# Kernel tuning notes

Hardware: AMD Instinct MI355X
Metric: run time of the kernel (lower is better)

## Reference

```python
import jax, jax.numpy as jnp
import numpy as np

B, R, C = 2, 64, 256
PH = PW = 7
KMAX = 8            # max pool-kernel size per axis given roi size bounds (kernel<=7 here)
HW = [160, 80, 40, 20]   # FPN level spatial sizes for a 640px image, strides 4/8/16/32
STRIDES = [4.0, 8.0, 16.0, 32.0]
TOP = 224.0         # config.top_pyramid_roi_size
HIDDEN = 2048
NCLS = 20
SCALE = float(np.round(np.sqrt(C), 2))  # np.round(sqrt(inner_dim),2) in SelfAttention


def setup_inputs() -> dict:
    key = jax.random.key(0)
    ks = jax.random.split(key, 32)
    U = lambda k, s, lo, hi: jax.random.uniform(k, s, minval=lo, maxval=hi)
    x1 = U(ks[0], (B, R), 0.0, 260.0)
    y1 = U(ks[1], (B, R), 0.0, 260.0)
    w = U(ks[2], (B, R), 16.0, 360.0)
    h = U(ks[3], (B, R), 16.0, 360.0)
    rois = jnp.stack([x1, y1, jnp.minimum(x1 + w, 639.0), jnp.minimum(y1 + h, 639.0)], -1)
    N = lambda k, s, sc: (sc * jax.random.normal(k, s)).astype(jnp.float32)
    inp = {'rois': rois}
    for i in range(4):
        inp[f'fm{i}'] = N(ks[4 + i], (B, C, HW[i], HW[i]), 1.0)
    inp['wq'] = N(ks[8], (C, C), 0.02);  inp['bq'] = jnp.zeros((C,), jnp.float32)
    inp['wk'] = N(ks[9], (C, C), 0.02);  inp['bk'] = jnp.zeros((C,), jnp.float32)
    inp['wv'] = N(ks[10], (C, C), 0.02); inp['bv'] = jnp.zeros((C,), jnp.float32)
    inp['wo'] = N(ks[11], (C, C), 0.02); inp['bo'] = jnp.zeros((C,), jnp.float32)
    inp['w1'] = N(ks[12], (C * PH * PW, HIDDEN), 0.02); inp['b1'] = jnp.zeros((HIDDEN,), jnp.float32)
    inp['w2'] = N(ks[13], (HIDDEN, HIDDEN), 0.02);       inp['b2'] = jnp.zeros((HIDDEN,), jnp.float32)
    inp['wreg'] = N(ks[14], (HIDDEN, 4 * (NCLS + 1)), 0.02); inp['breg'] = jnp.zeros((4 * (NCLS + 1),), jnp.float32)
    inp['wcls'] = N(ks[15], (HIDDEN, NCLS + 1), 0.02);       inp['bcls'] = jnp.zeros((NCLS + 1,), jnp.float32)
    return inp


def _forward(rois, fm0, fm1, fm2, fm3, wq, bq, wk, bk, wv, bv, wo, bo,
             w1, b1, w2, b2, wreg, breg, wcls, bcls):
    Hmax = HW[0]
    pad = lambda fm: jnp.pad(fm, ((0, 0), (0, 0), (0, Hmax - fm.shape[-2]), (0, Hmax - fm.shape[-1])))
    feats = jnp.stack([pad(fm0), pad(fm1), pad(fm2), pad(fm3)])  # [4,B,C,Hmax,Hmax]
    heights = jnp.array(HW, jnp.int32)
    strides = jnp.array(STRIDES, jnp.float32)

    r = rois.reshape(-1, 4)                 # [N,4] xyxy in pixels
    Nroi = r.shape[0]
    bidx = jnp.repeat(jnp.arange(B, dtype=jnp.int32), R)
    size = jnp.sqrt((r[:, 2] - r[:, 0]) * (r[:, 3] - r[:, 1]))
    # int() truncates toward zero, then clamp(0,3) -- matches torch
    lvl = jnp.clip((3.0 + jnp.log(size / TOP)).astype(jnp.int32), 0, 3)
    s = strides[lvl]
    x1 = (r[:, 0] / s).astype(jnp.int32); y1 = (r[:, 1] / s).astype(jnp.int32)
    x2 = (r[:, 2] / s).astype(jnp.int32); y2 = (r[:, 3] / s).astype(jnp.int32)
    Hl = heights[lvl]                        # per-roi level map size (square maps)

    def expand(lo, hi, cap, pool):
        # replicate the symmetric while-loop expansion until span >= pool
        for _ in range(pool):
            need = (hi - lo + 1) < pool
            lo = jnp.where(need, jnp.maximum(lo - 1, 0), lo)
            hi = jnp.where(need, jnp.minimum(hi + 1, cap - 1), hi)
        return lo, hi

    y1, y2 = expand(y1, y2, Hl, PH)
    x1, x2 = expand(x1, x2, Hl, PW)
    rh = y2 - y1 + 1; rw = x2 - x1 + 1
    kh = (rh + PH - 1) // PH; sh = rh // PH   # ceil / floor kernel & stride
    kw = (rw + PW - 1) // PW; sw = rw // PW

    ar_p = jnp.arange(PH); ar_k = jnp.arange(KMAX)

    def pool_one(l, b, yy, xx, kh_, kw_, sh_, sw_):
        rows = jnp.clip(yy + ar_p[:, None] * sh_ + ar_k[None, :], 0, Hmax - 1)  # [PH,K]
        cols = jnp.clip(xx + ar_p[:, None] * sw_ + ar_k[None, :], 0, Hmax - 1)  # [PW,K]
        patch = feats[l, b][:, rows[:, :, None, None], cols[None, None, :, :]]  # [C,PH,K,PW,K]
        m = (ar_k < kh_)[:, None, None] & (ar_k < kw_)[None, None, :]           # [K,1,K] -> bcast
        patch = jnp.where(m, patch, -jnp.inf)
        return patch.max(axis=(2, 4))                                           # [C,PH,PW]

    pooled = jax.vmap(pool_one)(lvl, bidx, y1, x1, kh, kw, sh, sw)  # [N,C,PH,PW]

    # SelfAttention over the PH*PW spatial tokens of each ROI
    L = PH * PW
    tok = pooled.reshape(Nroi, C, L).transpose(0, 2, 1)            # [N,L,C]
    q = tok @ wq + bq
    k = tok @ wk + bk
    v = tok @ wv + bv
    att = jax.nn.softmax(jnp.einsum('nlc,nmc->nlm', q, k) / SCALE, axis=-1)
    ctx = jnp.einsum('nlm,nmc->nlc', att, v) @ wo + bo             # [N,L,C]
    x = pooled.reshape(Nroi, C, L) + ctx.transpose(0, 2, 1)        # residual add
    x = x.reshape(Nroi, C * L)

    h1 = jax.nn.relu(x @ w1 + b1)
    h2 = jax.nn.relu(h1 @ w2 + b2)
    bbox_reg = h2 @ wreg + breg                                    # [N, 4*(NCLS+1)]
    bbox_classes = jax.nn.softmax(h2 @ wcls + bcls, axis=-1)       # [N, NCLS+1]
    return bbox_reg, bbox_classes


def reference(rois, fm0, fm1, fm2, fm3, wq, bq, wk, bk, wv, bv, wo, bo,
              w1, b1, w2, b2, wreg, breg, wcls, bcls):
    return _forward(rois, fm0, fm1, fm2, fm3, wq, bq, wk, bk, wv, bv, wo, bo,
                    w1, b1, w2, b2, wreg, breg, wcls, bcls)
```

## Files before the change

### kernel.cpp

```cpp
#include <hip/hip_runtime.h>
#include <hip/hip_bf16.h>
#include <stdint.h>

typedef __attribute__((ext_vector_type(8))) short bf16x8;
typedef __attribute__((ext_vector_type(4))) float f32x4;

__device__ __forceinline__ float blo(unsigned u){ union{float f;unsigned x;}v; v.x = u<<16; return v.f; }
__device__ __forceinline__ float bhi(unsigned u){ union{float f;unsigned x;}v; v.x = u & 0xFFFF0000u; return v.f; }
__device__ __forceinline__ unsigned short f2bf(float f){
  union{float f;unsigned x;}v; v.f=f; unsigned x=v.x;
  return (unsigned short)((x + 0x7fffu + ((x>>16)&1u)) >> 16);
}
__device__ __forceinline__ unsigned cvtpk(float lo, float hi){
  unsigned r;
  asm("v_cvt_pk_bf16_f32 %0, %1, %2" : "=v"(r) : "v"(lo), "v"(hi));
  return r;
}

__global__ __launch_bounds__(256) void pool_pack_kernel(
    const float* __restrict__ rois,
    const float* __restrict__ fm0, const float* __restrict__ fm1,
    const float* __restrict__ fm2, const float* __restrict__ fm3,
    float* __restrict__ pooled, unsigned short* __restrict__ tok,
    const float* __restrict__ wreg, const float* __restrict__ wcls, float* __restrict__ wT)
{
  int bx = blockIdx.x;
  int tid = threadIdx.x;
  if (bx >= 896){
    int c = bx - 896;
    if (c < 84){
      for (int k = tid; k < 2048; k += 256) wT[(size_t)c*2048 + k] = wreg[(size_t)k*84 + c];
    } else {
      int cc = c - 84;
      for (int k = tid; k < 2048; k += 256) wT[(size_t)c*2048 + k] = wcls[(size_t)k*21 + cc];
    }
    return;
  }
  int n = bx / 7;
  int ph = bx - n*7;
  int c = tid;
  const float* r = rois + n*4;
  int b = n >> 6;
  float rx1=r[0], ry1=r[1], rx2=r[2], ry2=r[3];
  float size = sqrtf((rx2-rx1)*(ry2-ry1));
  int lvl = (int)(3.0f + logf(size/224.0f));
  if (lvl < 0) lvl = 0; if (lvl > 3) lvl = 3;
  const float strides_[4] = {4.f,8.f,16.f,32.f};
  const int hw_[4] = {160,80,40,20};
  float s = strides_[lvl]; int Hl = hw_[lvl];
  int x1 = (int)(rx1/s), y1 = (int)(ry1/s), x2 = (int)(rx2/s), y2 = (int)(ry2/s);
  #pragma unroll
  for (int it=0; it<7; ++it){
    bool need = (y2-y1+1) < 7;
    if (need){ y1 = (y1-1 > 0) ? y1-1 : 0; y2 = (y2+1 < Hl-1) ? y2+1 : Hl-1; }
  }
  #pragma unroll
  for (int it=0; it<7; ++it){
    bool need = (x2-x1+1) < 7;
    if (need){ x1 = (x1-1 > 0) ? x1-1 : 0; x2 = (x2+1 < Hl-1) ? x2+1 : Hl-1; }
  }
  int rh = y2-y1+1, rw = x2-x1+1;
  int kh = (rh+6)/7, sh = rh/7, kw = (rw+6)/7, sw = rw/7;
  const float* fm = (lvl==0)?fm0:(lvl==1)?fm1:(lvl==2)?fm2:fm3;
  const float* fp = fm + ((size_t)(b*256 + c))*(size_t)(Hl*Hl);
  int r0 = y1 + ph*sh;
  for (int pw=0; pw<7; ++pw){
    int c0 = x1 + pw*sw;
    float m = -3.4e38f;
    for (int i=0;i<kh;++i){
      const float* rp = fp + (size_t)(r0+i)*Hl + c0;
      for (int j=0;j<kw;++j) m = fmaxf(m, rp[j]);
    }
    int l = ph*7+pw;
    pooled[((size_t)n*256 + c)*49 + l] = m;
    tok[((size_t)n*49 + l)*256 + c] = f2bf(m);
  }
}

template<int EPI>
__global__ __launch_bounds__(256) void gemm_kernel(
    const unsigned short* __restrict__ A,
    const float* __restrict__ B0, const float* __restrict__ B1, const float* __restrict__ B2,
    const float* __restrict__ bias0, const float* __restrict__ bias1, const float* __restrict__ bias2,
    unsigned short* __restrict__ o0, unsigned short* __restrict__ o1, unsigned short* __restrict__ o2,
    float* __restrict__ outf, const float* __restrict__ pooled,
    int M, int Nper, int K, int nM, int nN, int kChunk)
{
  __shared__ __align__(16) unsigned short Bs[2][2048];
  int per = nM*nN;
  int kc  = blockIdx.x / per;
  int rem = blockIdx.x - kc*per;
  int bm = rem % nM, bn = rem / nM;
  int m0 = bm*64, n0 = bn*64;
  int mat = n0 / Nper;
  int col0 = n0 - mat*Nper;
  const float* Bp    = (mat==0)?B0:(mat==1)?B1:B2;
  const float* biasp = (mat==0)?bias0:(mat==1)?bias1:bias2;
  unsigned short* outp = (mat==0)?o0:(mat==1)?o1:o2;
  int k0 = kc*kChunk;
  int nMacro = kChunk >> 7;
  int tid = threadIdx.x, lane = tid & 63, wave = tid >> 6;
  int wm = wave & 1, wn = wave >> 1;
  int g = lane >> 4, c = lane & 15;

  f32x4 acc[2][2];
  #pragma unroll
  for (int i=0;i<2;++i)
    #pragma unroll
    for (int j=0;j<2;++j){ acc[i][j][0]=0.f; acc[i][j][1]=0.f; acc[i][j][2]=0.f; acc[i][j][3]=0.f; }

  int brow = tid >> 3, bcg = tid & 7;
  int bw_idx = brow*64 + ((bcg*8) ^ ((brow>>3)<<4));
  const float* Bbase = Bp + (size_t)brow*Nper + col0 + bcg*8;
  int rb0 = g*512 + (((wn*2  )^g)*16 + c);
  int rb1 = g*512 + (((wn*2+1)^g)*16 + c);
  const unsigned short* Ap0 = A + (size_t)(m0 + wm*32 +      c)*K + g*8;
  const unsigned short* Ap1 = A + (size_t)(m0 + wm*32 + 16 + c)*K + g*8;

  auto writeB = [&](int buf, const float4& bx, const float4& by){
    uint4 w;
    w.x = cvtpk(bx.x,bx.y); w.y = cvtpk(bx.z,bx.w);
    w.z = cvtpk(by.x,by.y); w.w = cvtpk(by.z,by.w);
    *(uint4*)&Bs[buf][bw_idx] = w;
  };
  auto readFrags = [&](int buf, bf16x8& r0, bf16x8& r1){
    union { unsigned short s[8]; bf16x8 v; } u0, u1;
    const unsigned short* bsp = &Bs[buf][0];
    #pragma unroll
    for (int j=0;j<8;++j){ u0.s[j] = bsp[rb0 + j*64]; u1.s[j] = bsp[rb1 + j*64]; }
    r0 = u0.v; r1 = u1.v;
  };
  auto mfma4 = [&](const bf16x8& f0, const bf16x8& f1, const bf16x8& q0, const bf16x8& q1){
    acc[0][0] = __builtin_amdgcn_mfma_f32_16x16x32_bf16(f0,q0,acc[0][0],0,0,0);
    acc[0][1] = __builtin_amdgcn_mfma_f32_16x16x32_bf16(f0,q1,acc[0][1],0,0,0);
    acc[1][0] = __builtin_amdgcn_mfma_f32_16x16x32_bf16(f1,q0,acc[1][0],0,0,0);
    acc[1][1] = __builtin_amdgcn_mfma_f32_16x16x32_bf16(f1,q1,acc[1][1],0,0,0);
  };

  for (int mi = 0; mi < nMacro; ++mi){
    int kk = k0 + (mi << 7);
    uint4 a0x = *(const uint4*)(Ap0+kk),    a0y = *(const uint4*)(Ap1+kk);
    uint4 a1x = *(const uint4*)(Ap0+kk+32), a1y = *(const uint4*)(Ap1+kk+32);
    uint4 a2x = *(const uint4*)(Ap0+kk+64), a2y = *(const uint4*)(Ap1+kk+64);
    uint4 a3x = *(const uint4*)(Ap0+kk+96), a3y = *(const uint4*)(Ap1+kk+96);
    const float* p0 = Bbase + (size_t)kk*Nper;
    const float* p1 = p0 + (size_t)32*Nper;
    const float* p2 = p0 + (size_t)64*Nper;
    const float* p3 = p0 + (size_t)96*Nper;
    float4 b0a = *(const float4*)p0, b0b = *(const float4*)(p0+4);
    float4 b1a = *(const float4*)p1, b1b = *(const float4*)(p1+4);
    float4 b2a = *(const float4*)p2, b2b = *(const float4*)(p2+4);
    float4 b3a = *(const float4*)p3, b3b = *(const float4*)(p3+4);

    writeB(0, b0a, b0b);
    __syncthreads();

    bf16x8 q0,q1;
    readFrags(0,q0,q1);
    writeB(1,b1a,b1b);
    mfma4(*(const bf16x8*)&a0x, *(const bf16x8*)&a0y, q0,q1);
    __syncthreads();

    readFrags(1,q0,q1);
    writeB(0,b2a,b2b);
    mfma4(*(const bf16x8*)&a1x, *(const bf16x8*)&a1y, q0,q1);
    __syncthreads();

    readFrags(0,q0,q1);
    writeB(1,b3a,b3b);
    mfma4(*(const bf16x8*)&a2x, *(const bf16x8*)&a2y, q0,q1);
    __syncthreads();

    readFrags(1,q0,q1);
    mfma4(*(const bf16x8*)&a3x, *(const bf16x8*)&a3y, q0,q1);
  }

  int rq = g << 2, cl = c;
  #pragma unroll
  for (int mr=0;mr<2;++mr){
    #pragma unroll
    for (int nc=0;nc<2;++nc){
      int rowb = m0 + wm*32 + mr*16 + rq;
      int colM = col0 + wn*32 + nc*16 + cl;
      #pragma unroll
      for (int r2=0;r2<4;++r2){
        float v = acc[mr][nc][r2];
        int rr = rowb + r2;
        if constexpr (EPI==0){
          v += biasp[colM];
          outp[(size_t)rr*Nper + colM] = f2bf(v);
        } else if constexpr (EPI==1){
          v += biasp[colM];
          int nn = rr/49, l = rr - nn*49;
          v += pooled[((size_t)nn*256 + colM)*49 + l];
          outp[(size_t)nn*12544 + colM*49 + l] = f2bf(v);
        } else {
          outf[(size_t)kc*M*Nper + (size_t)rr*Nper + colM] = v;
        }
      }
    }
  }
}

__global__ __launch_bounds__(256) void reduce1_kernel(
    const float* __restrict__ part, const float* __restrict__ b1,
    unsigned short* __restrict__ h1, int nPart)
{
  int i = blockIdx.x*256 + threadIdx.x;
  float4 s = ((const float4*)part)[i];
  for (int kc = 1; kc < nPart; ++kc){
    float4 p = ((const float4*)part)[(size_t)kc*65536 + i];
    s.x += p.x; s.y += p.y; s.z += p.z; s.w += p.w;
  }
  float4 bb = *(const float4*)(b1 + ((i<<2) & 2047));
  s.x = fmaxf(s.x+bb.x,0.f); s.y = fmaxf(s.y+bb.y,0.f);
  s.z = fmaxf(s.z+bb.z,0.f); s.w = fmaxf(s.w+bb.w,0.f);
  uint2 w;
  w.x = cvtpk(s.x, s.y); w.y = cvtpk(s.z, s.w);
  *(uint2*)&h1[(size_t)i<<2] = w;
}

__global__ __launch_bounds__(256) void reduce2_kernel(
    const float* __restrict__ part, float* __restrict__ h2f, int nPart)
{
  int i = blockIdx.x*256 + threadIdx.x;
  float4 s = ((const float4*)part)[i];
  for (int kc = 1; kc < nPart; ++kc){
    float4 p = ((const float4*)part)[(size_t)kc*65536 + i];
    s.x += p.x; s.y += p.y; s.z += p.z; s.w += p.w;
  }
  ((float4*)h2f)[i] = s;
}

__global__ __launch_bounds__(256) void attn_kernel(
    const unsigned short* __restrict__ Q, const unsigned short* __restrict__ Km,
    const unsigned short* __restrict__ V, unsigned short* __restrict__ ctx)
{
  int n = blockIdx.x, half = blockIdx.y, tid = threadIdx.x;
  int r0 = half*25, rcnt = half ? 24 : 25;
  __shared__ __align__(16) unsigned short qs[25*256];
  __shared__ __align__(16) unsigned short ks[49*260];
  __shared__ float S[25*49];
  const uint4* qg = (const uint4*)(Q + ((size_t)n*49 + r0)*256);
  for (int i = tid; i < rcnt*32; i += 256) ((uint4*)qs)[i] = qg[i];
  const uint2* kg = (const uint2*)(Km + (size_t)n*49*256);
  for (int i = tid; i < 49*64; i += 256){
    int j = i >> 6, s = i & 63;
    *(uint2*)(ks + j*260 + s*4) = kg[i];
  }
  __syncthreads();
  for (int p = tid; p < rcnt*49; p += 256){
    int i = p/49, j = p - i*49;
    const uint2* qr = (const uint2*)(qs + i*256);
    const uint2* kr = (const uint2*)(ks + j*260);
    float sum = 0.f;
    #pragma unroll 8
    for (int c4 = 0; c4 < 64; ++c4){
      uint2 qv = qr[c4], kv = kr[c4];
      sum += blo(qv.x)*blo(kv.x) + bhi(qv.x)*bhi(kv.x);
      sum += blo(qv.y)*blo(kv.y) + bhi(qv.y)*bhi(kv.y);
    }
    S[p] = sum * (1.0f/16.0f);
  }
  __syncthreads();
  const uint2* vg = (const uint2*)(V + (size_t)n*49*256);
  for (int i = tid; i < 49*64; i += 256){
    int j = i >> 6, s = i & 63;
    *(uint2*)(ks + j*260 + s*4) = vg[i];
  }
  if (tid < rcnt){
    float* row = S + tid*49;
    float mx = row[0];
    for (int j=1;j<49;++j) mx = fmaxf(mx,row[j]);
    float sm = 0.f;
    for (int j=0;j<49;++j){ float e = expf(row[j]-mx); row[j]=e; sm+=e; }
    float inv = 1.0f/sm;
    for (int j=0;j<49;++j) row[j] *= inv;
  }
  __syncthreads();
  for (int idx = tid; idx < rcnt*64; idx += 256){
    int i = idx >> 6, cp4 = idx & 63;
    const float* att = S + i*49;
    float s0=0.f, s1=0.f, s2=0.f, s3=0.f;
    #pragma unroll 7
    for (int j=0;j<49;++j){
      uint2 v = *(const uint2*)(ks + j*260 + cp4*4);
      float a = att[j];
      s0 += a*blo(v.x); s1 += a*bhi(v.x);
      s2 += a*blo(v.y); s3 += a*bhi(v.y);
    }
    uint2 outw;
    outw.x = (unsigned)f2bf(s0) | ((unsigned)f2bf(s1) << 16);
    outw.y = (unsigned)f2bf(s2) | ((unsigned)f2bf(s3) << 16);
    *(uint2*)&ctx[((size_t)n*49 + r0 + i)*256 + cp4*4] = outw;
  }
}

__global__ __launch_bounds__(256) void heads_dot(
    const float* __restrict__ h2f, const float* __restrict__ b2,
    const float* __restrict__ wT,
    const float* __restrict__ breg, const float* __restrict__ bcls,
    float* __restrict__ out, float* __restrict__ logits)
{
  int gw = (blockIdx.x*256 + threadIdx.x) >> 6;
  int lane = threadIdx.x & 63;
  int m = gw / 105, c = gw - m*105;
  const float4* hp = (const float4*)(h2f + (size_t)m*2048);
  const float4* bp = (const float4*)b2;
  const float4* wp = (const float4*)(wT + (size_t)c*2048);
  float sum = 0.f;
  #pragma unroll
  for (int i=0;i<8;++i){
    float4 a = hp[i*64 + lane];
    float4 bb = bp[i*64 + lane];
    float4 w = wp[i*64 + lane];
    sum += fmaxf(a.x+bb.x,0.f)*w.x + fmaxf(a.y+bb.y,0.f)*w.y
         + fmaxf(a.z+bb.z,0.f)*w.z + fmaxf(a.w+bb.w,0.f)*w.w;
  }
  #pragma unroll
  for (int off=32; off; off>>=1) sum += __shfl_down(sum, off, 64);
  if (lane == 0){
    if (c < 84) out[(size_t)m*84 + c] = sum + breg[c];
    else        logits[(size_t)m*21 + (c-84)] = sum + bcls[c-84];
  }
}

__global__ __launch_bounds__(128) void cls_softmax(
    const float* __restrict__ logits, float* __restrict__ out)
{
  int m = threadIdx.x;
  const float* lg = logits + (size_t)m*21;
  float mx = lg[0];
  #pragma unroll
  for (int j=1;j<21;++j) mx = fmaxf(mx, lg[j]);
  float sm = 0.f;
  float e[21];
  #pragma unroll
  for (int j=0;j<21;++j){ e[j] = expf(lg[j]-mx); sm += e[j]; }
  float inv = 1.0f/sm;
  #pragma unroll
  for (int j=0;j<21;++j) out[10752 + (size_t)m*21 + j] = e[j]*inv;
}

extern "C" void kernel_launch(void* const* d_in, const int* in_sizes, int n_in,
                              void* d_out, int out_size, void* d_ws, size_t ws_size,
                              hipStream_t stream)
{
  (void)in_sizes; (void)n_in; (void)out_size; (void)ws_size;
  const float* rois = (const float*)d_in[0];
  const float* fm0  = (const float*)d_in[1];
  const float* fm1  = (const float*)d_in[2];
  const float* fm2  = (const float*)d_in[3];
  const float* fm3  = (const float*)d_in[4];
  const float* wq   = (const float*)d_in[5];
  const float* bq   = (const float*)d_in[6];
  const float* wk   = (const float*)d_in[7];
  const float* bk   = (const float*)d_in[8];
  const float* wv   = (const float*)d_in[9];
  const float* bv   = (const float*)d_in[10];
  const float* wo   = (const float*)d_in[11];
  const float* bo   = (const float*)d_in[12];
  const float* w1   = (const float*)d_in[13];
  const float* b1   = (const float*)d_in[14];
  const float* w2   = (const float*)d_in[15];
  const float* b2   = (const float*)d_in[16];
  const float* wreg = (const float*)d_in[17];
  const float* breg = (const float*)d_in[18];
  const float* wcls = (const float*)d_in[19];
  const float* bcls = (const float*)d_in[20];
  float* out = (float*)d_out;

  char* ws = (char*)d_ws;
  float*          pooled = (float*)(ws + 0);
  unsigned short* tok    = (unsigned short*)(ws + 6422528);
  unsigned short* Qb     = (unsigned short*)(ws + 9633792);
  unsigned short* Kb     = (unsigned short*)(ws + 12845056);
  unsigned short* Vb     = (unsigned short*)(ws + 16056320);
  unsigned short* ctx    = (unsigned short*)(ws + 19267584);
  unsigned short* xb     = (unsigned short*)(ws + 22478848);
  float*          h2f    = (float*)(ws + 25690112);
  unsigned short* h1     = (unsigned short*)(ws + 26738688);
  float*          wT     = (float*)(ws + 27787264);
  float*          logits = (float*)(ws + 28647424);
  float*          h1part = (float*)(ws + 0);
  float*          h2part = (float*)(ws + 0);

  pool_pack_kernel<<<1001,256,0,stream>>>(rois, fm0, fm1, fm2, fm3, pooled, tok,
                                          wreg, wcls, wT);

  gemm_kernel<0><<<1176,256,0,stream>>>(tok, wq,wk,wv, bq,bk,bv,
                                        Qb,Kb,Vb, nullptr, nullptr, 6272,256,256, 98,12, 256);

  attn_kernel<<<dim3(128,2),256,0,stream>>>(Qb, Kb, Vb, ctx);

  gemm_kernel<1><<<392,256,0,stream>>>(ctx, wo,wo,wo, bo,bo,bo,
                                       xb,xb,xb, nullptr, pooled, 6272,256,256, 98,4, 256);

  gemm_kernel<2><<<896,256,0,stream>>>(xb, w1,w1,w1, nullptr,nullptr,nullptr,
                                       nullptr,nullptr,nullptr, h1part, nullptr,
                                       128,2048,12544, 2,32, 896);
  reduce1_kernel<<<256,256,0,stream>>>(h1part, b1, h1, 14);

  gemm_kernel<2><<<1024,256,0,stream>>>(h1, w2,w2,w2, nullptr,nullptr,nullptr,
                                        nullptr,nullptr,nullptr, h2part, nullptr,
                                        128,2048,2048, 2,32, 128);
  reduce2_kernel<<<256,256,0,stream>>>(h2part, h2f, 16);

  heads_dot<<<3360,256,0,stream>>>(h2f, b2, wT, breg, bcls, out, logits);
  cls_softmax<<<1,128,0,stream>>>(logits, out);
}
```

Baseline: 189.2 us.

## Pre-pack w1/w2 into swizzled bf16 tiles before the MLP GEMMs

```diff
diff --git a/kernel.cpp b/kernel.cpp
--- a/kernel.cpp
+++ b/kernel.cpp
@@ -22,10 +22,33 @@
     const float* __restrict__ fm0, const float* __restrict__ fm1,
     const float* __restrict__ fm2, const float* __restrict__ fm3,
     float* __restrict__ pooled, unsigned short* __restrict__ tok,
-    const float* __restrict__ wreg, const float* __restrict__ wcls, float* __restrict__ wT)
+    const float* __restrict__ wreg, const float* __restrict__ wcls, float* __restrict__ wT,
+    const float* __restrict__ w1c, unsigned short* __restrict__ w1p,
+    const float* __restrict__ w2c, unsigned short* __restrict__ w2p)
 {
   int bx = blockIdx.x;
   int tid = threadIdx.x;
+  if (bx >= 1001){
+    int cb = bx - 1001;
+    const float* W; unsigned short* P; int kb, Kp;
+    if (cb < 1568){ W = w1c; P = w1p; kb = cb*8;          Kp = 392; }
+    else          { W = w2c; P = w2p; kb = (cb-1568)*8;   Kp = 64;  }
+    int k  = kb + (tid>>5);
+    int bn = tid & 31;
+    int kr = k & 31, k32 = k >> 5;
+    const float4* src = (const float4*)(W + (size_t)k*2048 + bn*64);
+    uint4* dst = (uint4*)(P + ((size_t)bn*Kp + k32)*2048 + (size_t)kr*64);
+    int sw = (kr>>3)<<1;
+    #pragma unroll
+    for (int bcg=0; bcg<8; ++bcg){
+      float4 a = src[bcg*2], b = src[bcg*2+1];
+      uint4 w;
+      w.x = cvtpk(a.x,a.y); w.y = cvtpk(a.z,a.w);
+      w.z = cvtpk(b.x,b.y); w.w = cvtpk(b.z,b.w);
+      dst[bcg ^ sw] = w;
+    }
+    return;
+  }
   if (bx >= 896){
     int c = bx - 896;
     if (c < 84){
@@ -60,12 +83,12 @@
     if (need){ x1 = (x1-1 > 0) ? x1-1 : 0; x2 = (x2+1 < Hl-1) ? x2+1 : Hl-1; }
   }
   int rh = y2-y1+1, rw = x2-x1+1;
-  int kh = (rh+6)/7, sh = rh/7, kw = (rw+6)/7, sw = rw/7;
+  int kh = (rh+6)/7, sh = rh/7, kw = (rw+6)/7, sw2 = rw/7;
   const float* fm = (lvl==0)?fm0:(lvl==1)?fm1:(lvl==2)?fm2:fm3;
   const float* fp = fm + ((size_t)(b*256 + c))*(size_t)(Hl*Hl);
   int r0 = y1 + ph*sh;
   for (int pw=0; pw<7; ++pw){
-    int c0 = x1 + pw*sw;
+    int c0 = x1 + pw*sw2;
     float m = -3.4e38f;
     for (int i=0;i<kh;++i){
       const float* rp = fp + (size_t)(r0+i)*Hl + c0;
@@ -77,10 +100,11 @@
   }
 }
 
-template<int EPI>
+template<int EPI, int BSRC>
 __global__ __launch_bounds__(256) void gemm_kernel(
     const unsigned short* __restrict__ A,
     const float* __restrict__ B0, const float* __restrict__ B1, const float* __restrict__ B2,
+    const unsigned short* __restrict__ Bpre,
     const float* __restrict__ bias0, const float* __restrict__ bias1, const float* __restrict__ bias2,
     unsigned short* __restrict__ o0, unsigned short* __restrict__ o1, unsigned short* __restrict__ o2,
     float* __restrict__ outf, const float* __restrict__ pooled,
@@ -112,16 +136,20 @@
   int brow = tid >> 3, bcg = tid & 7;
   int bw_idx = brow*64 + ((bcg*8) ^ ((brow>>3)<<4));
   const float* Bbase = Bp + (size_t)brow*Nper + col0 + bcg*8;
+  const unsigned short* Pbase = Bpre + (size_t)bn*(K>>5)*2048 + tid*8;
   int rb0 = g*512 + (((wn*2  )^g)*16 + c);
   int rb1 = g*512 + (((wn*2+1)^g)*16 + c);
   const unsigned short* Ap0 = A + (size_t)(m0 + wm*32 +      c)*K + g*8;
   const unsigned short* Ap1 = A + (size_t)(m0 + wm*32 + 16 + c)*K + g*8;
 
-  auto writeB = [&](int buf, const float4& bx, const float4& by){
+  auto writeBf32 = [&](int buf, const float4& bx, const float4& by){
     uint4 w;
     w.x = cvtpk(bx.x,bx.y); w.y = cvtpk(bx.z,bx.w);
     w.z = cvtpk(by.x,by.y); w.w = cvtpk(by.z,by.w);
     *(uint4*)&Bs[buf][bw_idx] = w;
+  };
+  auto writeBpre = [&](int buf, const uint4& v){
+    *(uint4*)&Bs[buf][tid*8] = v;
   };
   auto readFrags = [&](int buf, bf16x8& r0, bf16x8& r1){
     union { unsigned short s[8]; bf16x8 v; } u0, u1;
@@ -143,31 +171,42 @@
     uint4 a1x = *(const uint4*)(Ap0+kk+32), a1y = *(const uint4*)(Ap1+kk+32);
     uint4 a2x = *(const uint4*)(Ap0+kk+64), a2y = *(const uint4*)(Ap1+kk+64);
     uint4 a3x = *(const uint4*)(Ap0+kk+96), a3y = *(const uint4*)(Ap1+kk+96);
-    const float* p0 = Bbase + (size_t)kk*Nper;
-    const float* p1 = p0 + (size_t)32*Nper;
-    const float* p2 = p0 + (size_t)64*Nper;
-    const float* p3 = p0 + (size_t)96*Nper;
-    float4 b0a = *(const float4*)p0, b0b = *(const float4*)(p0+4);
-    float4 b1a = *(const float4*)p1, b1b = *(const float4*)(p1+4);
-    float4 b2a = *(const float4*)p2, b2b = *(const float4*)(p2+4);
-    float4 b3a = *(const float4*)p3, b3b = *(const float4*)(p3+4);
-
-    writeB(0, b0a, b0b);
+
+    float4 b0a,b0b,b1a,b1b,b2a,b2b,b3a,b3b;
+    uint4 v0,v1,v2,v3;
+    if constexpr (BSRC==0){
+      const float* p0 = Bbase + (size_t)kk*Nper;
+      const float* p1 = p0 + (size_t)32*Nper;
+      const float* p2 = p0 + (size_t)64*Nper;
+      const float* p3 = p0 + (size_t)96*Nper;
+      b0a = *(const float4*)p0; b0b = *(const float4*)(p0+4);
+      b1a = *(const float4*)p1; b1b = *(const float4*)(p1+4);
+      b2a = *(const float4*)p2; b2b = *(const float4*)(p2+4);
+      b3a = *(const float4*)p3; b3b = *(const float4*)(p3+4);
+    } else {
+      const unsigned short* q = Pbase + (size_t)(kk>>5)*2048;
+      v0 = *(const uint4*)q;
+      v1 = *(const uint4*)(q + 2048);
+      v2 = *(const uint4*)(q + 4096);
+      v3 = *(const uint4*)(q + 6144);
+    }
+
+    if constexpr (BSRC==0) writeBf32(0,b0a,b0b); else writeBpre(0,v0);
     __syncthreads();
 
     bf16x8 q0,q1;
     readFrags(0,q0,q1);
-    writeB(1,b1a,b1b);
+    if constexpr (BSRC==0) writeBf32(1,b1a,b1b); else writeBpre(1,v1);
     mfma4(*(const bf16x8*)&a0x, *(const bf16x8*)&a0y, q0,q1);
     __syncthreads();
 
     readFrags(1,q0,q1);
-    writeB(0,b2a,b2b);
+    if constexpr (BSRC==0) writeBf32(0,b2a,b2b); else writeBpre(0,v2);
     mfma4(*(const bf16x8*)&a1x, *(const bf16x8*)&a1y, q0,q1);
     __syncthreads();
 
     readFrags(0,q0,q1);
-    writeB(1,b3a,b3b);
+    if constexpr (BSRC==0) writeBf32(1,b3a,b3b); else writeBpre(1,v3);
     mfma4(*(const bf16x8*)&a2x, *(const bf16x8*)&a2y, q0,q1);
     __syncthreads();
 
@@ -346,7 +385,7 @@
                               void* d_out, int out_size, void* d_ws, size_t ws_size,
                               hipStream_t stream)
 {
-  (void)in_sizes; (void)n_in; (void)out_size; (void)ws_size;
+  (void)in_sizes; (void)n_in; (void)out_size;
   const float* rois = (const float*)d_in[0];
   const float* fm0  = (const float*)d_in[1];
   const float* fm1  = (const float*)d_in[2];
@@ -382,29 +421,43 @@
   unsigned short* h1     = (unsigned short*)(ws + 26738688);
   float*          wT     = (float*)(ws + 27787264);
   float*          logits = (float*)(ws + 28647424);
+  unsigned short* w1p    = (unsigned short*)(ws + 29360128);
+  unsigned short* w2p    = (unsigned short*)(ws + 80740352);
   float*          h1part = (float*)(ws + 0);
   float*          h2part = (float*)(ws + 0);
 
-  pool_pack_kernel<<<1001,256,0,stream>>>(rois, fm0, fm1, fm2, fm3, pooled, tok,
-                                          wreg, wcls, wT);
-
-  gemm_kernel<0><<<1176,256,0,stream>>>(tok, wq,wk,wv, bq,bk,bv,
-                                        Qb,Kb,Vb, nullptr, nullptr, 6272,256,256, 98,12, 256);
+  bool big = ws_size >= (size_t)90*1024*1024;
+
+  pool_pack_kernel<<<(big ? 2825 : 1001),256,0,stream>>>(
+      rois, fm0, fm1, fm2, fm3, pooled, tok, wreg, wcls, wT, w1, w1p, w2, w2p);
+
+  gemm_kernel<0,0><<<1176,256,0,stream>>>(tok, wq,wk,wv, nullptr, bq,bk,bv,
+                                          Qb,Kb,Vb, nullptr, nullptr, 6272,256,256, 98,12, 256);
 
   attn_kernel<<<dim3(128,2),256,0,stream>>>(Qb, Kb, Vb, ctx);
 
-  gemm_kernel<1><<<392,256,0,stream>>>(ctx, wo,wo,wo, bo,bo,bo,
-                                       xb,xb,xb, nullptr, pooled, 6272,256,256, 98,4, 256);
-
-  gemm_kernel<2><<<896,256,0,stream>>>(xb, w1,w1,w1, nullptr,nullptr,nullptr,
-                                       nullptr,nullptr,nullptr, h1part, nullptr,
-                                       128,2048,12544, 2,32, 896);
-  reduce1_kernel<<<256,256,0,stream>>>(h1part, b1, h1, 14);
-
-  gemm_kernel<2><<<1024,256,0,stream>>>(h1, w2,w2,w2, nullptr,nullptr,nullptr,
-                                        nullptr,nullptr,nullptr, h2part, nullptr,
-                                        128,2048,2048, 2,32, 128);
-  reduce2_kernel<<<256,256,0,stream>>>(h2part, h2f, 16);
+  gemm_kernel<1,0><<<392,256,0,stream>>>(ctx, wo,wo,wo, nullptr, bo,bo,bo,
+                                         xb,xb,xb, nullptr, pooled, 6272,256,256, 98,4, 256);
+
+  if (big){
+    gemm_kernel<2,1><<<896,256,0,stream>>>(xb, nullptr,nullptr,nullptr, w1p,
+                                           nullptr,nullptr,nullptr, nullptr,nullptr,nullptr,
+                                           h1part, nullptr, 128,2048,12544, 2,32, 896);
+    reduce1_kernel<<<256,256,0,stream>>>(h1part, b1, h1, 14);
+    gemm_kernel<2,1><<<1024,256,0,stream>>>(h1, nullptr,nullptr,nullptr, w2p,
+                                            nullptr,nullptr,nullptr, nullptr,nullptr,nullptr,
+                                            h2part, nullptr, 128,2048,2048, 2,32, 128);
+    reduce2_kernel<<<256,256,0,stream>>>(h2part, h2f, 16);
+  } else {
+    gemm_kernel<2,0><<<896,256,0,stream>>>(xb, w1,w1,w1, nullptr, nullptr,nullptr,nullptr,
+                                           nullptr,nullptr,nullptr, h1part, nullptr,
+                                           128,2048,12544, 2,32, 896);
+    reduce1_kernel<<<256,256,0,stream>>>(h1part, b1, h1, 14);
+    gemm_kernel<2,0><<<1024,256,0,stream>>>(h1, w2,w2,w2, nullptr, nullptr,nullptr,nullptr,
+                                            nullptr,nullptr,nullptr, h2part, nullptr,
+                                            128,2048,2048, 2,32, 128);
+    reduce2_kernel<<<256,256,0,stream>>>(h2part, h2f, 16);
+  }
 
   heads_dot<<<3360,256,0,stream>>>(h2f, b2, wT, breg, bcls, out, logits);
   cls_softmax<<<1,128,0,stream>>>(logits, out);
```

New measurement: 227.1 us. +20.1%, slower.
